# Kernel optimization log

Measured on AMD Instinct MI355X. Metric: run time of the kernel, lower is better.

## Reference

```python
import jax, jax.numpy as jnp
import numpy as np

SCALE = 25.0        # surrogate-gradient sharpness
SPIKE_REG = 0.01
TARGET_RATE = 0.5


@jax.custom_vjp
def spike_fn(membrane, threshold):
    # Heaviside forward, fast-sigmoid surrogate backward (matches torch autograd.Function)
    return (membrane >= threshold).astype(membrane.dtype)


def _spike_fwd(membrane, threshold):
    return spike_fn(membrane, threshold), (membrane, threshold)


def _spike_bwd(res, g):
    membrane, threshold = res
    gm = g / (SCALE * jnp.abs(membrane - threshold) + 1.0) ** 2
    # torch returns None for threshold grad from the surrogate function
    return gm, jnp.zeros_like(threshold)


spike_fn.defvjp(_spike_fwd, _spike_bwd)


def lif(x, threshold, tau_raw, timesteps):
    tau = jax.nn.sigmoid(tau_raw)
    input_current = x / timesteps

    def step(carry, _):
        membrane, spike_sum = carry
        membrane = tau * membrane + input_current
        spikes = spike_fn(membrane, threshold)
        membrane = membrane - spikes * threshold  # soft reset
        return (membrane, spike_sum + spikes), None

    init = (jnp.zeros_like(x), jnp.zeros_like(x))
    (membrane, spike_sum), _ = jax.lax.scan(step, init, None, length=timesteps)

    firing_rate = spike_sum.mean() / timesteps
    reg_loss = SPIKE_REG * (firing_rate - TARGET_RATE) ** 2
    return spike_sum, membrane, reg_loss


def setup_inputs() -> dict:
    key = jax.random.key(0)
    x = jax.random.normal(key, (32, 256, 4096), dtype=jnp.float32)
    return {
        "x": x,
        "threshold": jnp.asarray(1.0, dtype=jnp.float32),
        "tau": jnp.asarray(0.75, dtype=jnp.float32),
        "timesteps": 8,
    }


def reference(x, threshold, tau, timesteps):
    return lif(x, threshold, tau, timesteps)
```

## Files before the change

### kernel.cpp

```cpp
#include <hip/hip_runtime.h>
#include <math.h>

typedef float f32x4 __attribute__((ext_vector_type(4)));

#ifndef USE_FMA
#define USE_FMA 0
#endif

__device__ __forceinline__ float step_madd(float tau, float m, float ic) {
#if USE_FMA
    return __fmaf_rn(tau, m, ic);
#else
    return __fadd_rn(__fmul_rn(tau, m), ic);
#endif
}

template <int TT>
__device__ __forceinline__ void lif_elem(float ic, float tau, float thr, int T,
                                         float& m_out, int& s_out) {
    float m = 0.0f;
    int s = 0;
    if (TT > 0) {
#pragma unroll
        for (int t = 0; t < TT; ++t) {
            m = step_madd(tau, m, ic);
            if (m >= thr) { m = __fsub_rn(m, thr); ++s; }
        }
    } else {
        for (int t = 0; t < T; ++t) {
            m = step_madd(tau, m, ic);
            if (m >= thr) { m = __fsub_rn(m, thr); ++s; }
        }
    }
    m_out = m;
    s_out = s;
}

__global__ __launch_bounds__(256) void lif_fwd(
    const f32x4* __restrict__ x4,
    const float* __restrict__ thr_p,
    const float* __restrict__ tau_p,
    const int* __restrict__ ts_p,
    f32x4* __restrict__ ssum4,
    f32x4* __restrict__ mem4,
    unsigned int* __restrict__ total_spikes,
    int n4)
{
    const float thr  = thr_p[0];
    const float traw = tau_p[0];
    const int   T    = ts_p[0];

    const float e   = expf(-traw);
    const float tau = __fdiv_rn(1.0f, __fadd_rn(1.0f, e));
    const float tF  = (float)T;

    unsigned int cnt = 0;
    const int stride = gridDim.x * blockDim.x;
    for (int i = blockIdx.x * blockDim.x + threadIdx.x; i < n4; i += stride) {
        const f32x4 xv = x4[i];
        float ic[4];
#pragma unroll
        for (int j = 0; j < 4; ++j) ic[j] = __fdiv_rn(xv[j], tF);

        float m[4];
        int   s[4];
        if (T == 8) {
#pragma unroll
            for (int j = 0; j < 4; ++j) lif_elem<8>(ic[j], tau, thr, T, m[j], s[j]);
        } else {
#pragma unroll
            for (int j = 0; j < 4; ++j) lif_elem<0>(ic[j], tau, thr, T, m[j], s[j]);
        }

        f32x4 sv = { (float)s[0], (float)s[1], (float)s[2], (float)s[3] };
        f32x4 mv = { m[0], m[1], m[2], m[3] };
        __builtin_nontemporal_store(sv, &ssum4[i]);
        __builtin_nontemporal_store(mv, &mem4[i]);
        cnt += (unsigned int)(s[0] + s[1] + s[2] + s[3]);
    }

    int c = (int)cnt;
    for (int off = 32; off > 0; off >>= 1)
        c += __shfl_down(c, off, 64);
    __shared__ unsigned int wred[4];
    const int lane = threadIdx.x & 63;
    const int wid  = threadIdx.x >> 6;
    if (lane == 0) wred[wid] = (unsigned int)c;
    __syncthreads();
    if (threadIdx.x == 0)
        atomicAdd(total_spikes, wred[0] + wred[1] + wred[2] + wred[3]);
}

__global__ void lif_finalize(const unsigned int* __restrict__ total_spikes,
                             const int* __restrict__ ts_p,
                             float* __restrict__ reg_out,
                             long long n)
{
    const int T = ts_p[0];
    const double mean_d = (double)(*total_spikes) / (double)n;
    const float meanf = (float)mean_d;
    const float rate  = __fdiv_rn(meanf, (float)T);
    const float d     = __fsub_rn(rate, 0.5f);
    reg_out[0] = __fmul_rn(0.01f, __fmul_rn(d, d));
}

extern "C" void kernel_launch(void* const* d_in, const int* in_sizes, int n_in,
                              void* d_out, int out_size, void* d_ws, size_t ws_size,
                              hipStream_t stream) {
    const float* x   = (const float*)d_in[0];
    const float* thr = (const float*)d_in[1];
    const float* tau = (const float*)d_in[2];
    const int*   ts  = (const int*)d_in[3];
    const int N  = in_sizes[0];
    const int n4 = N / 4;

    float* ssum = (float*)d_out;
    float* mem  = ssum + (size_t)N;
    float* reg  = ssum + (size_t)2 * N;
    unsigned int* total = (unsigned int*)d_ws;

    (void)hipMemsetAsync(d_ws, 0, sizeof(unsigned int), stream);

    const int block = 256;
    int grid = 2048;
    const int needed = (n4 + block - 1) / block;
    if (needed < grid) grid = needed;

    hipLaunchKernelGGL(lif_fwd, dim3(grid), dim3(block), 0, stream,
                       (const f32x4*)x, thr, tau, ts,
                       (f32x4*)ssum, (f32x4*)mem, total, n4);
    hipLaunchKernelGGL(lif_finalize, dim3(1), dim3(1), 0, stream,
                       total, ts, reg, (long long)N);
}
```

Baseline: 373.3 us.

## Drop memset and atomic via per-block partials; branchless vectorized LIF update

Replaces the memset plus global atomic counter with per-block float partial sums that a 256-thread finalize kernel reduces in double, removing one stream operation. The per-element LIF loop becomes branchless f32x4 vector math using an fma for the soft reset. Division by T is replaced with multiplication by its reciprocal when T is a power of two. A scalar tail path is added for element counts that are not a multiple of four. The kernel is memory-bound, so the arithmetic changes likely matter less than removing the memset.

```diff
diff --git a/kernel.cpp b/kernel.cpp
--- a/kernel.cpp
+++ b/kernel.cpp
@@ -3,33 +3,34 @@
 
 typedef float f32x4 __attribute__((ext_vector_type(4)));
 
-#ifndef USE_FMA
-#define USE_FMA 0
-#endif
-
-__device__ __forceinline__ float step_madd(float tau, float m, float ic) {
-#if USE_FMA
-    return __fmaf_rn(tau, m, ic);
-#else
-    return __fadd_rn(__fmul_rn(tau, m), ic);
-#endif
-}
-
 template <int TT>
-__device__ __forceinline__ void lif_elem(float ic, float tau, float thr, int T,
-                                         float& m_out, int& s_out) {
-    float m = 0.0f;
-    int s = 0;
+__device__ __forceinline__ void lif4(const f32x4 ic, const float tau, const float thr,
+                                     const int T, f32x4& m_out, f32x4& s_out) {
+#pragma clang fp contract(off)
+    f32x4 m = {0.0f, 0.0f, 0.0f, 0.0f};
+    f32x4 s = {0.0f, 0.0f, 0.0f, 0.0f};
+    const f32x4 tau4  = {tau, tau, tau, tau};
+    const f32x4 nthr4 = {-thr, -thr, -thr, -thr};
     if (TT > 0) {
 #pragma unroll
         for (int t = 0; t < TT; ++t) {
-            m = step_madd(tau, m, ic);
-            if (m >= thr) { m = __fsub_rn(m, thr); ++s; }
+            const f32x4 p = tau4 * m;
+            m = p + ic;
+            f32x4 sp;
+#pragma unroll
+            for (int j = 0; j < 4; ++j) sp[j] = (m[j] >= thr) ? 1.0f : 0.0f;
+            m = __builtin_elementwise_fma(nthr4, sp, m);
+            s = s + sp;
         }
     } else {
         for (int t = 0; t < T; ++t) {
-            m = step_madd(tau, m, ic);
-            if (m >= thr) { m = __fsub_rn(m, thr); ++s; }
+            const f32x4 p = tau4 * m;
+            m = p + ic;
+            f32x4 sp;
+#pragma unroll
+            for (int j = 0; j < 4; ++j) sp[j] = (m[j] >= thr) ? 1.0f : 0.0f;
+            m = __builtin_elementwise_fma(nthr4, sp, m);
+            s = s + sp;
         }
     }
     m_out = m;
@@ -37,15 +38,16 @@
 }
 
 __global__ __launch_bounds__(256) void lif_fwd(
-    const f32x4* __restrict__ x4,
+    const float* __restrict__ x,
     const float* __restrict__ thr_p,
     const float* __restrict__ tau_p,
     const int* __restrict__ ts_p,
-    f32x4* __restrict__ ssum4,
-    f32x4* __restrict__ mem4,
-    unsigned int* __restrict__ total_spikes,
-    int n4)
+    float* __restrict__ ssum,
+    float* __restrict__ mem,
+    float* __restrict__ partials,
+    int n4, int ntail)
 {
+#pragma clang fp contract(off)
     const float thr  = thr_p[0];
     const float traw = tau_p[0];
     const int   T    = ts_p[0];
@@ -53,55 +55,84 @@
     const float e   = expf(-traw);
     const float tau = __fdiv_rn(1.0f, __fadd_rn(1.0f, e));
     const float tF  = (float)T;
+    const bool  pw2 = T > 0 && (T & (T - 1)) == 0;
+    const float rT  = __fdiv_rn(1.0f, tF);
 
-    unsigned int cnt = 0;
+    const f32x4* __restrict__ x4 = (const f32x4*)x;
+    f32x4* __restrict__ ssum4 = (f32x4*)ssum;
+    f32x4* __restrict__ mem4  = (f32x4*)mem;
+
+    float cnt = 0.0f;
+    const int gtid   = blockIdx.x * blockDim.x + threadIdx.x;
     const int stride = gridDim.x * blockDim.x;
-    for (int i = blockIdx.x * blockDim.x + threadIdx.x; i < n4; i += stride) {
+
+    if (gtid < ntail) {
+        const int idx = n4 * 4 + gtid;
+        const float icv = pw2 ? __fmul_rn(x[idx], rT) : __fdiv_rn(x[idx], tF);
+        float m = 0.0f, sf = 0.0f;
+        for (int t = 0; t < T; ++t) {
+            m = __fadd_rn(__fmul_rn(tau, m), icv);
+            if (m >= thr) { m = __fsub_rn(m, thr); sf += 1.0f; }
+        }
+        ssum[idx] = sf; mem[idx] = m; cnt += sf;
+    }
+
+    const f32x4 rT4 = {rT, rT, rT, rT};
+    for (int i = gtid; i < n4; i += stride) {
         const f32x4 xv = x4[i];
-        float ic[4];
-#pragma unroll
-        for (int j = 0; j < 4; ++j) ic[j] = __fdiv_rn(xv[j], tF);
-
-        float m[4];
-        int   s[4];
-        if (T == 8) {
-#pragma unroll
-            for (int j = 0; j < 4; ++j) lif_elem<8>(ic[j], tau, thr, T, m[j], s[j]);
+        f32x4 ic;
+        if (pw2) {
+            ic = xv * rT4;
         } else {
 #pragma unroll
-            for (int j = 0; j < 4; ++j) lif_elem<0>(ic[j], tau, thr, T, m[j], s[j]);
+            for (int j = 0; j < 4; ++j) ic[j] = __fdiv_rn(xv[j], tF);
         }
 
-        f32x4 sv = { (float)s[0], (float)s[1], (float)s[2], (float)s[3] };
-        f32x4 mv = { m[0], m[1], m[2], m[3] };
-        __builtin_nontemporal_store(sv, &ssum4[i]);
-        __builtin_nontemporal_store(mv, &mem4[i]);
-        cnt += (unsigned int)(s[0] + s[1] + s[2] + s[3]);
+        f32x4 m, s;
+        if (T == 8) lif4<8>(ic, tau, thr, T, m, s);
+        else        lif4<0>(ic, tau, thr, T, m, s);
+
+        __builtin_nontemporal_store(s, &ssum4[i]);
+        __builtin_nontemporal_store(m, &mem4[i]);
+        cnt += s[0] + s[1] + s[2] + s[3];
     }
 
-    int c = (int)cnt;
+    float c = cnt;
     for (int off = 32; off > 0; off >>= 1)
         c += __shfl_down(c, off, 64);
-    __shared__ unsigned int wred[4];
+    __shared__ float wred[4];
     const int lane = threadIdx.x & 63;
     const int wid  = threadIdx.x >> 6;
-    if (lane == 0) wred[wid] = (unsigned int)c;
+    if (lane == 0) wred[wid] = c;
     __syncthreads();
     if (threadIdx.x == 0)
-        atomicAdd(total_spikes, wred[0] + wred[1] + wred[2] + wred[3]);
+        partials[blockIdx.x] = wred[0] + wred[1] + wred[2] + wred[3];
 }
 
-__global__ void lif_finalize(const unsigned int* __restrict__ total_spikes,
-                             const int* __restrict__ ts_p,
-                             float* __restrict__ reg_out,
-                             long long n)
+__global__ __launch_bounds__(256) void lif_finalize(
+    const float* __restrict__ partials, int nparts,
+    const int* __restrict__ ts_p,
+    float* __restrict__ reg_out, long long n)
 {
     const int T = ts_p[0];
-    const double mean_d = (double)(*total_spikes) / (double)n;
-    const float meanf = (float)mean_d;
-    const float rate  = __fdiv_rn(meanf, (float)T);
-    const float d     = __fsub_rn(rate, 0.5f);
-    reg_out[0] = __fmul_rn(0.01f, __fmul_rn(d, d));
+    double acc = 0.0;
+    for (int i = threadIdx.x; i < nparts; i += 256)
+        acc += (double)partials[i];
+    for (int off = 32; off > 0; off >>= 1)
+        acc += __shfl_down(acc, off, 64);
+    __shared__ double dred[4];
+    const int lane = threadIdx.x & 63;
+    const int wid  = threadIdx.x >> 6;
+    if (lane == 0) dred[wid] = acc;
+    __syncthreads();
+    if (threadIdx.x == 0) {
+        const double total  = dred[0] + dred[1] + dred[2] + dred[3];
+        const double mean_d = total / (double)n;
+        const float  meanf  = (float)mean_d;
+        const float  rate   = __fdiv_rn(meanf, (float)T);
+        const float  d      = __fsub_rn(rate, 0.5f);
+        reg_out[0] = __fmul_rn(0.01f, __fmul_rn(d, d));
+    }
 }
 
 extern "C" void kernel_launch(void* const* d_in, const int* in_sizes, int n_in,
@@ -111,24 +142,22 @@
     const float* thr = (const float*)d_in[1];
     const float* tau = (const float*)d_in[2];
     const int*   ts  = (const int*)d_in[3];
-    const int N  = in_sizes[0];
-    const int n4 = N / 4;
+    const int N     = in_sizes[0];
+    const int n4    = N / 4;
+    const int ntail = N - n4 * 4;
 
     float* ssum = (float*)d_out;
     float* mem  = ssum + (size_t)N;
     float* reg  = ssum + (size_t)2 * N;
-    unsigned int* total = (unsigned int*)d_ws;
-
-    (void)hipMemsetAsync(d_ws, 0, sizeof(unsigned int), stream);
+    float* partials = (float*)d_ws;
 
     const int block = 256;
-    int grid = 2048;
-    const int needed = (n4 + block - 1) / block;
-    if (needed < grid) grid = needed;
+    int grid = (n4 + block - 1) / block;
+    if (grid > 2048) grid = 2048;
+    if (grid < 1)    grid = 1;
 
     hipLaunchKernelGGL(lif_fwd, dim3(grid), dim3(block), 0, stream,
-                       (const f32x4*)x, thr, tau, ts,
-                       (f32x4*)ssum, (f32x4*)mem, total, n4);
-    hipLaunchKernelGGL(lif_finalize, dim3(1), dim3(1), 0, stream,
-                       total, ts, reg, (long long)N);
+                       x, thr, tau, ts, ssum, mem, partials, n4, ntail);
+    hipLaunchKernelGGL(lif_finalize, dim3(1), dim3(block), 0, stream,
+                       partials, grid, ts, reg, (long long)N);
 }
```

Measured after the change: 371.5 us. Within noise of the previous version (-0.5%).
